# Kernel tuning notes

Hardware: AMD Instinct MI355X
Metric: run time of the kernel (lower is better)

Reference implementation:

```python
import jax, jax.numpy as jnp
import numpy as np
from jax import lax

SIGMA = 3.0
AP_CUT = 15


def _gauss_kernel(sigma, truncate=4.0):
    r = int(truncate * sigma + 0.5)
    x = np.arange(-r, r + 1, dtype=np.float32)
    k = np.exp(-0.5 * (x / sigma) ** 2)
    return jnp.asarray(k / k.sum()), r

KERN, RAD = _gauss_kernel(SIGMA)


def _smooth(f):
    """Separable Gaussian smoothing; circular on y (DV), replicate on x (AP).
    f: [..., Y, X] -> same shape."""
    lead = f.shape[:-2]
    Y, X = f.shape[-2:]
    g = f.reshape((-1, 1, Y, X))
    g = jnp.pad(g, ((0, 0), (0, 0), (RAD, RAD), (0, 0)), mode='wrap')
    g = jnp.pad(g, ((0, 0), (0, 0), (0, 0), (RAD, RAD)), mode='edge')
    ky = KERN.reshape(1, 1, -1, 1)
    kx = KERN.reshape(1, 1, 1, -1)
    g = lax.conv_general_dilated(g, ky, (1, 1), 'VALID')
    g = lax.conv_general_dilated(g, kx, (1, 1), 'VALID')
    return g.reshape(lead + (Y, X))


def _gradient(f):
    """Covariant gradient: Gaussian smooth then central differences.
    Returns [..., Y, X, 2] with index 0 = d/dy (circular), 1 = d/dx (replicate)."""
    g = _smooth(f)
    dy = 0.5 * (jnp.roll(g, -1, axis=-2) - jnp.roll(g, 1, axis=-2))
    gp = jnp.pad(g, [(0, 0)] * (g.ndim - 1) + [(1, 1)], mode='edge')
    dx = 0.5 * (gp[..., 2:] - gp[..., :-2])
    return jnp.stack([dy, dx], axis=-1)


def _postprocess(f):
    f = f.at[..., :AP_CUT].set(0.0)
    f = f.at[..., -AP_CUT:].set(0.0)
    return _smooth(f)


def setup_inputs() -> dict:
    key = jax.random.key(0)
    k1, k2 = jax.random.split(key)
    Y, X = 1024, 2048
    y = 0.1 * jax.random.normal(k1, (5, Y, X), dtype=jnp.float32)
    v = 0.1 * jax.random.normal(k2, (2, Y, X), dtype=jnp.float32)
    return {"y": y, "v": v}


def reference(y, v):
    Y, X = y.shape[-2:]
    # InputProcessor.transform: split state into 2x2 tensor m and scalar s
    m = y[:4].reshape(2, 2, Y, X)
    s = y[4]

    # get_velocity: left-right symmetrization (flip DV axis, negate y-component)
    v_lr = jnp.flip(v, axis=-2)
    v_lr = v_lr.at[0].multiply(-1.0)
    v = 0.5 * (v + v_lr)

    d1_m = _gradient(m)          # [2,2,Y,X,2]
    d1_s = _gradient(s)          # [Y,X,2]
    d1_v = _gradient(v)          # [2,Y,X,2]

    sdot = -jnp.einsum('iyx,yxi->yx', v, d1_s)

    T = jnp.transpose(d1_v, (0, 3, 1, 2))       # iyxj -> ijyx
    Tt = jnp.transpose(T, (1, 0, 2, 3))
    O = -0.5 * (T - Tt)                         # vorticity
    E = 0.5 * (T + Tt)                          # strain rate

    lhs = jnp.einsum('kyx,ijyxk->ijyx', v, d1_m)
    lhs = lhs + jnp.einsum('ikyx,kjyx->ijyx', O, m)
    lhs = lhs - jnp.einsum('ikyx,kjyx->ijyx', m, O)

    # rhs_eCad reaction terms
    trm = jnp.einsum('kkyx->yx', m)
    trE = jnp.einsum('kkyx->yx', E)
    gamma_dv = jnp.array([[1.0, 0.0], [0.0, 0.0]], dtype=y.dtype)[..., None, None]
    rhs = -(0.11 - 0.099 * s) * m
    rhs = rhs + (0.767 + 0.055 * s) * m * trE
    rhs = rhs + (0.732 - 0.59 * s) * trm * m
    rhs = rhs + (0.069 - 0.048 * s) * trm * gamma_dv

    mdot = _postprocess(-lhs + rhs)
    sdot = _postprocess(sdot)

    # inverse_transform: stack back into 5-channel state derivative
    return jnp.concatenate([mdot.reshape(4, Y, X), sdot[None]], axis=0)
```

## Files before the change

### kernel.cpp

```cpp
#include <hip/hip_runtime.h>
#include <math.h>

#define Y_ 1024
#define X_ 2048
#define YX_ (Y_*X_)
#define RAD_ 12
#define NT_ 25
#define ND_ 27
#define APC_ 15
#define PAD_ 16

struct W25 { float w[NT_]; };
struct D27 { float d[ND_]; };

__device__ __forceinline__ void wconv4(const float wb[36], const W25& W, float wc[4]) {
#pragma unroll
  for (int j = 0; j < 4; ++j) {
    float s = 0.f;
#pragma unroll
    for (int t = 0; t < NT_; ++t) s += W.w[t] * wb[4 + j + t];
    wc[j] = s;
  }
}
__device__ __forceinline__ void dconv4(const float wb[36], const D27& D, float dc[4]) {
#pragma unroll
  for (int j = 0; j < 4; ++j) {
    float s = 0.f;
#pragma unroll
    for (int t = 0; t < ND_; ++t) s += D.d[t] * wb[3 + j + t];
    dc[j] = s;
  }
}
__device__ __forceinline__ void load9(float wb[36], const float* p) {
#pragma unroll
  for (int i = 0; i < 9; ++i) {
    float4 t = *(const float4*)(p + 4 * i);
    wb[4*i+0] = t.x; wb[4*i+1] = t.y; wb[4*i+2] = t.z; wb[4*i+3] = t.w;
  }
}

__global__ __launch_bounds__(256) void ksmooth_y7c(
    const float* __restrict__ yin, const float* __restrict__ vin,
    float* __restrict__ out, W25 W)
{
  const int id = blockIdx.x;
  const int w  = (id & 7) * 112 + (id >> 3);
  const int yg = w % 64, xh = (w / 64) & 1, z = w / 128;
  const int y0 = yg * 16;
  const int xo = xh * 1024 + threadIdx.x * 4;

  float4 acc[16];
#pragma unroll
  for (int j = 0; j < 16; ++j) acc[j] = make_float4(0.f, 0.f, 0.f, 0.f);

  if (z < 5) {
    const float* base = yin + z * YX_;
#pragma unroll
    for (int g = 0; g < 4; ++g) {
      float4 b[10];
#pragma unroll
      for (int i = 0; i < 10; ++i) {
        const int r = (y0 - RAD_ + 10*g + i + Y_) & (Y_ - 1);
        b[i] = *(const float4*)(base + r * X_ + xo);
      }
#pragma unroll
      for (int i = 0; i < 10; ++i) {
        const int t = 10*g + i;
#pragma unroll
        for (int j = 0; j < 16; ++j) {
          const int k = t - j;
          if (k >= 0 && k < NT_) {
            const float wk = W.w[k];
            acc[j].x += wk * b[i].x; acc[j].y += wk * b[i].y;
            acc[j].z += wk * b[i].z; acc[j].w += wk * b[i].w;
          }
        }
      }
    }
  } else {
    const int   c   = z - 5;
    const float sgn = (c == 0) ? -1.f : 1.f;
    const float* base = vin + c * YX_;
#pragma unroll
    for (int g = 0; g < 8; ++g) {
      float4 a5[5], b5[5];
#pragma unroll
      for (int i = 0; i < 5; ++i) {
        const int r = (y0 - RAD_ + 5*g + i + Y_) & (Y_ - 1);
        a5[i] = *(const float4*)(base + r * X_ + xo);
        b5[i] = *(const float4*)(base + (Y_ - 1 - r) * X_ + xo);
      }
#pragma unroll
      for (int i = 0; i < 5; ++i) {
        const int t = 5*g + i;
        float4 val;
        val.x = 0.5f * (a5[i].x + sgn * b5[i].x);
        val.y = 0.5f * (a5[i].y + sgn * b5[i].y);
        val.z = 0.5f * (a5[i].z + sgn * b5[i].z);
        val.w = 0.5f * (a5[i].w + sgn * b5[i].w);
#pragma unroll
        for (int j = 0; j < 16; ++j) {
          const int k = t - j;
          if (k >= 0 && k < NT_) {
            const float wk = W.w[k];
            acc[j].x += wk * val.x; acc[j].y += wk * val.y;
            acc[j].z += wk * val.z; acc[j].w += wk * val.w;
          }
        }
      }
    }
  }
#pragma unroll
  for (int j = 0; j < 16; ++j)
    *(float4*)(out + z * YX_ + (y0 + j) * X_ + xo) = acc[j];
}

__global__ __launch_bounds__(256) void kderiv2(
    const float* __restrict__ gY, const float* __restrict__ vin,
    float* __restrict__ F, W25 W, D27 D)
{
  const int id = blockIdx.x;
  const int w  = (id & 7) * 224 + (id >> 3);
  const int yg = w % 128, xh = (w / 128) & 1, z = w / 256;
  const int y0 = yg * 8;
  const int x0 = xh * 1024 + threadIdx.x * 4;

  float w2[4], w1[4], dcp[4];
#pragma unroll
  for (int j = 0; j < 4; ++j) { w2[j] = 0.f; w1[j] = 0.f; dcp[j] = 0.f; }

  if (z < 5) {
    const float* base = gY + z * YX_;
#pragma unroll
    for (int r = 0; r < 10; ++r) {
      const int ry = (y0 - 1 + r + Y_) & (Y_ - 1);
      float wb[36];
      load9(wb, base + ry * X_ + x0 - 16);
      float wc[4]; wconv4(wb, W, wc);
      float dc[4];
      if (r >= 1 && r <= 8) dconv4(wb, D, dc);
      else { dc[0]=dc[1]=dc[2]=dc[3]=0.f; }
      if (r >= 2) {
        const int t = r - 2, ty = y0 + t;
        float4 a  = *(const float4*)(vin + 0*YX_ + ty * X_ + x0);
        float4 bm = *(const float4*)(vin + 0*YX_ + (Y_-1-ty) * X_ + x0);
        float4 c  = *(const float4*)(vin + 1*YX_ + ty * X_ + x0);
        float4 dm = *(const float4*)(vin + 1*YX_ + (Y_-1-ty) * X_ + x0);
        const float v0[4] = {0.5f*(a.x-bm.x), 0.5f*(a.y-bm.y),
                             0.5f*(a.z-bm.z), 0.5f*(a.w-bm.w)};
        const float v1[4] = {0.5f*(c.x+dm.x), 0.5f*(c.y+dm.y),
                             0.5f*(c.z+dm.z), 0.5f*(c.w+dm.w)};
        float4 o;
        o.x = v0[0]*(0.5f*(wc[0]-w2[0])) + v1[0]*dcp[0];
        o.y = v0[1]*(0.5f*(wc[1]-w2[1])) + v1[1]*dcp[1];
        o.z = v0[2]*(0.5f*(wc[2]-w2[2])) + v1[2]*dcp[2];
        o.w = v0[3]*(0.5f*(wc[3]-w2[3])) + v1[3]*dcp[3];
        *(float4*)(F + z * YX_ + ty * X_ + x0) = o;
      }
#pragma unroll
      for (int j = 0; j < 4; ++j) { w2[j] = w1[j]; w1[j] = wc[j]; dcp[j] = dc[j]; }
    }
  } else if (z == 5) {
    const float* b5 = gY + 5 * YX_;
    const float* b6 = gY + 6 * YX_;
#pragma unroll
    for (int r = 0; r < 10; ++r) {
      const int ry = (y0 - 1 + r + Y_) & (Y_ - 1);
      float wb[36];
      load9(wb, b6 + ry * X_ + x0 - 16);
      float wc[4]; wconv4(wb, W, wc);
      float dc[4];
      if (r >= 1 && r <= 8) {
        float wb5[36];
        load9(wb5, b5 + ry * X_ + x0 - 16);
        dconv4(wb5, D, dc);
      } else { dc[0]=dc[1]=dc[2]=dc[3]=0.f; }
      if (r >= 2) {
        const int t = r - 2, ty = y0 + t;
        float4 o;
        o.x = -0.5f*(dcp[0] - 0.5f*(wc[0]-w2[0]));
        o.y = -0.5f*(dcp[1] - 0.5f*(wc[1]-w2[1]));
        o.z = -0.5f*(dcp[2] - 0.5f*(wc[2]-w2[2]));
        o.w = -0.5f*(dcp[3] - 0.5f*(wc[3]-w2[3]));
        *(float4*)(F + 5 * YX_ + ty * X_ + x0) = o;
      }
#pragma unroll
      for (int j = 0; j < 4; ++j) { w2[j] = w1[j]; w1[j] = wc[j]; dcp[j] = dc[j]; }
    }
  } else {
    const float* b5 = gY + 5 * YX_;
    const float* b6 = gY + 6 * YX_;
#pragma unroll
    for (int r = 0; r < 10; ++r) {
      const int ry = (y0 - 1 + r + Y_) & (Y_ - 1);
      float wb[36];
      load9(wb, b5 + ry * X_ + x0 - 16);
      float wc[4]; wconv4(wb, W, wc);
      float dc[4];
      if (r >= 1 && r <= 8) {
        float wb6[36];
        load9(wb6, b6 + ry * X_ + x0 - 16);
        dconv4(wb6, D, dc);
      } else { dc[0]=dc[1]=dc[2]=dc[3]=0.f; }
      if (r >= 2) {
        const int t = r - 2, ty = y0 + t;
        float4 o;
        o.x = dcp[0] + 0.5f*(wc[0]-w2[0]);
        o.y = dcp[1] + 0.5f*(wc[1]-w2[1]);
        o.z = dcp[2] + 0.5f*(wc[2]-w2[2]);
        o.w = dcp[3] + 0.5f*(wc[3]-w2[3]);
        *(float4*)(F + 6 * YX_ + ty * X_ + x0) = o;
      }
#pragma unroll
      for (int j = 0; j < 4; ++j) { w2[j] = w1[j]; w1[j] = wc[j]; dcp[j] = dc[j]; }
    }
  }
}

__global__ __launch_bounds__(256) void kcombine(
    const float* __restrict__ F, const float* __restrict__ yin,
    float* __restrict__ B)
{
  const int yy = blockIdx.y;
  const int x0 = (blockIdx.x * 256 + threadIdx.x) * 4;

  if (x0 < RAD_ || x0 > X_ - PAD_) {
#pragma unroll
    for (int zc = 0; zc < 5; ++zc)
      *(float4*)(B + zc * YX_ + yy * X_ + x0) = make_float4(0.f,0.f,0.f,0.f);
    return;
  }

  float adv[5][4];
#pragma unroll
  for (int c = 0; c < 5; ++c) {
    float4 t = *(const float4*)(F + c * YX_ + yy * X_ + x0);
    adv[c][0] = t.x; adv[c][1] = t.y; adv[c][2] = t.z; adv[c][3] = t.w;
  }
  float4 wv  = *(const float4*)(F + 5 * YX_ + yy * X_ + x0);
  float4 tev = *(const float4*)(F + 6 * YX_ + yy * X_ + x0);
  const float wa[4]  = {wv.x, wv.y, wv.z, wv.w};
  const float tea[4] = {tev.x, tev.y, tev.z, tev.w};

  float rm[5][4];
#pragma unroll
  for (int zc = 0; zc < 5; ++zc) {
    float4 t = *(const float4*)(yin + zc * YX_ + yy * X_ + x0);
    rm[zc][0] = t.x; rm[zc][1] = t.y; rm[zc][2] = t.z; rm[zc][3] = t.w;
  }

  float o[5][4];
#pragma unroll
  for (int j = 0; j < 4; ++j) {
    const float m00r = rm[0][j], m01r = rm[1][j], m10r = rm[2][j], m11r = rm[3][j];
    const float sr   = rm[4][j];
    const float w_   = wa[j];
    const float trE  = tea[j];
    const float trm  = m00r + m11r;

    const float lhs00 = adv[0][j] + w_ * (m10r + m01r);
    const float lhs01 = adv[1][j] + w_ * (m11r - m00r);
    const float lhs10 = adv[2][j] + w_ * (m11r - m00r);
    const float lhs11 = adv[3][j] - w_ * (m01r + m10r);

    const float f  = -(0.11f - 0.099f * sr)
                   + (0.767f + 0.055f * sr) * trE
                   + (0.732f - 0.59f  * sr) * trm;
    const float cd = (0.069f - 0.048f * sr) * trm;
    const float sd = -adv[4][j];

    const int   xg   = x0 + j;
    const float mask = (xg < APC_ || xg >= X_ - APC_) ? 0.f : 1.f;
    o[0][j] = mask * (f * m00r + cd - lhs00);
    o[1][j] = mask * (f * m01r      - lhs01);
    o[2][j] = mask * (f * m10r      - lhs10);
    o[3][j] = mask * (f * m11r      - lhs11);
    o[4][j] = mask * sd;
  }
#pragma unroll
  for (int zc = 0; zc < 5; ++zc)
    *(float4*)(B + zc * YX_ + yy * X_ + x0) =
        make_float4(o[zc][0], o[zc][1], o[zc][2], o[zc][3]);
}

__global__ __launch_bounds__(256) void kxsmooth(
    const float* __restrict__ in, float* __restrict__ out, W25 W)
{
  const int z  = blockIdx.z;
  const int yy = blockIdx.y;
  const int x0 = (blockIdx.x * 256 + threadIdx.x) * 4;
  const float* row = in + z * YX_ + yy * X_;

  float buf[28];
  if (x0 >= RAD_ && x0 + 4 + RAD_ <= X_) {
#pragma unroll
    for (int i = 0; i < 7; ++i) {
      float4 t = *(const float4*)(row + x0 - RAD_ + 4 * i);
      buf[4*i+0] = t.x; buf[4*i+1] = t.y; buf[4*i+2] = t.z; buf[4*i+3] = t.w;
    }
  } else {
#pragma unroll
    for (int i = 0; i < 28; ++i) {
      int xx = x0 - RAD_ + i;
      xx = xx < 0 ? 0 : (xx > X_ - 1 ? X_ - 1 : xx);
      buf[i] = row[xx];
    }
  }
  float a0 = 0.f, a1 = 0.f, a2 = 0.f, a3 = 0.f;
#pragma unroll
  for (int t = 0; t < NT_; ++t) {
    const float wk = W.w[t];
    a0 += wk * buf[t + 0];
    a1 += wk * buf[t + 1];
    a2 += wk * buf[t + 2];
    a3 += wk * buf[t + 3];
  }
  *(float4*)(out + z * YX_ + yy * X_ + x0) = make_float4(a0, a1, a2, a3);
}

__global__ __launch_bounds__(256) void ksmooth_y5c(
    const float* __restrict__ in, float* __restrict__ out, W25 W)
{
  const int id = blockIdx.x;
  const int w  = (id & 7) * 80 + (id >> 3);
  const int yg = w % 64, xh = (w / 64) & 1, z = w / 128;
  const int y0 = yg * 16;
  const int xo = xh * 1024 + threadIdx.x * 4;
  const float* base = in + z * YX_;

  float4 acc[16];
#pragma unroll
  for (int j = 0; j < 16; ++j) acc[j] = make_float4(0.f, 0.f, 0.f, 0.f);

#pragma unroll
  for (int g = 0; g < 4; ++g) {
    float4 b[10];
#pragma unroll
    for (int i = 0; i < 10; ++i) {
      const int r = (y0 - RAD_ + 10*g + i + Y_) & (Y_ - 1);
      b[i] = *(const float4*)(base + r * X_ + xo);
    }
#pragma unroll
    for (int i = 0; i < 10; ++i) {
      const int t = 10*g + i;
#pragma unroll
      for (int j = 0; j < 16; ++j) {
        const int k = t - j;
        if (k >= 0 && k < NT_) {
          const float wk = W.w[k];
          acc[j].x += wk * b[i].x; acc[j].y += wk * b[i].y;
          acc[j].z += wk * b[i].z; acc[j].w += wk * b[i].w;
        }
      }
    }
  }
#pragma unroll
  for (int j = 0; j < 16; ++j)
    *(float4*)(out + z * YX_ + (y0 + j) * X_ + xo) = acc[j];
}

extern "C" void kernel_launch(void* const* d_in, const int* in_sizes, int n_in,
                              void* d_out, int out_size, void* d_ws, size_t ws_size,
                              hipStream_t stream)
{
  const float* yin = (const float*)d_in[0];
  const float* vin = (const float*)d_in[1];
  float* out = (float*)d_out;

  float* gY = (float*)d_ws + PAD_;
  float* F  = gY + 7 * (size_t)YX_;
  float* B  = F;
  float* C  = gY;

  W25 W; D27 D;
  double wd[NT_], s = 0.0;
  for (int i = 0; i < NT_; ++i) {
    const double x = i - RAD_;
    wd[i] = exp(-0.5 * (x / 3.0) * (x / 3.0));
    s += wd[i];
  }
  for (int i = 0; i < NT_; ++i) W.w[i] = (float)(wd[i] / s);
  for (int t = 0; t < ND_; ++t) {
    const double a = (t - 2 >= 0 && t - 2 < NT_) ? wd[t - 2] / s : 0.0;
    const double b = (t < NT_) ? wd[t] / s : 0.0;
    D.d[t] = (float)(0.5 * (a - b));
  }

  ksmooth_y7c<<<896, 256, 0, stream>>>(yin, vin, gY, W);
  kderiv2    <<<1792, 256, 0, stream>>>(gY, vin, F, W, D);
  kcombine   <<<dim3(2, 1024), 256, 0, stream>>>(F, yin, B);
  kxsmooth   <<<dim3(2, 1024, 5), 256, 0, stream>>>(B, C, W);
  ksmooth_y5c<<<640, 256, 0, stream>>>(C, out, W);
}
```

Baseline: 251.8 us.

## Fuse derivative and combine kernels into one per-row kernel

Merges the derivative kernel (kderiv2) and the combine kernel into a single kernel. Each thread now computes the x-smoothing and central differences for all seven channels directly from the y-smoothed buffer, instead of writing the intermediate F buffer and reading it back. This removes one launch and a full 7-channel intermediate round trip through memory. In exchange it recomputes the x-convolution for three rows per output row (up, down, centre) rather than sliding them along a row window, so arithmetic and redundant loads go up.

```diff
diff --git a/kernel.cpp b/kernel.cpp
--- a/kernel.cpp
+++ b/kernel.cpp
@@ -6,37 +6,55 @@
 #define YX_ (Y_*X_)
 #define RAD_ 12
 #define NT_ 25
-#define ND_ 27
 #define APC_ 15
 #define PAD_ 16
 
 struct W25 { float w[NT_]; };
-struct D27 { float d[ND_]; };
-
-__device__ __forceinline__ void wconv4(const float wb[36], const W25& W, float wc[4]) {
-#pragma unroll
-  for (int j = 0; j < 4; ++j) {
-    float s = 0.f;
-#pragma unroll
-    for (int t = 0; t < NT_; ++t) s += W.w[t] * wb[4 + j + t];
-    wc[j] = s;
-  }
-}
-__device__ __forceinline__ void dconv4(const float wb[36], const D27& D, float dc[4]) {
-#pragma unroll
-  for (int j = 0; j < 4; ++j) {
-    float s = 0.f;
-#pragma unroll
-    for (int t = 0; t < ND_; ++t) s += D.d[t] * wb[3 + j + t];
-    dc[j] = s;
-  }
-}
+
 __device__ __forceinline__ void load9(float wb[36], const float* p) {
 #pragma unroll
   for (int i = 0; i < 9; ++i) {
     float4 t = *(const float4*)(p + 4 * i);
     wb[4*i+0] = t.x; wb[4*i+1] = t.y; wb[4*i+2] = t.z; wb[4*i+3] = t.w;
   }
+}
+
+__device__ __forceinline__ void derivs_ch(
+    const float* __restrict__ base, int yy, int yu, int yd, int x0,
+    const W25& W, float dX[4], float dY[4])
+{
+  float wb[36];
+  load9(wb, base + yy * X_ + x0 - 16);
+  float wc6[6];
+#pragma unroll
+  for (int jj = 0; jj < 6; ++jj) {
+    float s = 0.f;
+#pragma unroll
+    for (int t = 0; t < NT_; ++t) s += W.w[t] * wb[3 + jj + t];
+    wc6[jj] = s;
+  }
+#pragma unroll
+  for (int j = 0; j < 4; ++j) dX[j] = 0.5f * (wc6[j + 2] - wc6[j]);
+
+  float au[4], ad[4];
+  load9(wb, base + yu * X_ + x0 - 16);
+#pragma unroll
+  for (int j = 0; j < 4; ++j) {
+    float s = 0.f;
+#pragma unroll
+    for (int t = 0; t < NT_; ++t) s += W.w[t] * wb[4 + j + t];
+    au[j] = s;
+  }
+  load9(wb, base + yd * X_ + x0 - 16);
+#pragma unroll
+  for (int j = 0; j < 4; ++j) {
+    float s = 0.f;
+#pragma unroll
+    for (int t = 0; t < NT_; ++t) s += W.w[t] * wb[4 + j + t];
+    ad[j] = s;
+  }
+#pragma unroll
+  for (int j = 0; j < 4; ++j) dY[j] = 0.5f * (au[j] - ad[j]);
 }
 
 __global__ __launch_bounds__(256) void ksmooth_y7c(
@@ -115,114 +133,18 @@
     *(float4*)(out + z * YX_ + (y0 + j) * X_ + xo) = acc[j];
 }
 
-__global__ __launch_bounds__(256) void kderiv2(
-    const float* __restrict__ gY, const float* __restrict__ vin,
-    float* __restrict__ F, W25 W, D27 D)
+__global__ __launch_bounds__(256) void kfused(
+    const float* __restrict__ gY,
+    const float* __restrict__ yin,
+    const float* __restrict__ vin,
+    float* __restrict__ B,
+    W25 W)
 {
   const int id = blockIdx.x;
-  const int w  = (id & 7) * 224 + (id >> 3);
-  const int yg = w % 128, xh = (w / 128) & 1, z = w / 256;
-  const int y0 = yg * 8;
+  const int w  = (id & 7) * 256 + (id >> 3);
+  const int yy = w & (Y_ - 1);
+  const int xh = w >> 10;
   const int x0 = xh * 1024 + threadIdx.x * 4;
-
-  float w2[4], w1[4], dcp[4];
-#pragma unroll
-  for (int j = 0; j < 4; ++j) { w2[j] = 0.f; w1[j] = 0.f; dcp[j] = 0.f; }
-
-  if (z < 5) {
-    const float* base = gY + z * YX_;
-#pragma unroll
-    for (int r = 0; r < 10; ++r) {
-      const int ry = (y0 - 1 + r + Y_) & (Y_ - 1);
-      float wb[36];
-      load9(wb, base + ry * X_ + x0 - 16);
-      float wc[4]; wconv4(wb, W, wc);
-      float dc[4];
-      if (r >= 1 && r <= 8) dconv4(wb, D, dc);
-      else { dc[0]=dc[1]=dc[2]=dc[3]=0.f; }
-      if (r >= 2) {
-        const int t = r - 2, ty = y0 + t;
-        float4 a  = *(const float4*)(vin + 0*YX_ + ty * X_ + x0);
-        float4 bm = *(const float4*)(vin + 0*YX_ + (Y_-1-ty) * X_ + x0);
-        float4 c  = *(const float4*)(vin + 1*YX_ + ty * X_ + x0);
-        float4 dm = *(const float4*)(vin + 1*YX_ + (Y_-1-ty) * X_ + x0);
-        const float v0[4] = {0.5f*(a.x-bm.x), 0.5f*(a.y-bm.y),
-                             0.5f*(a.z-bm.z), 0.5f*(a.w-bm.w)};
-        const float v1[4] = {0.5f*(c.x+dm.x), 0.5f*(c.y+dm.y),
-                             0.5f*(c.z+dm.z), 0.5f*(c.w+dm.w)};
-        float4 o;
-        o.x = v0[0]*(0.5f*(wc[0]-w2[0])) + v1[0]*dcp[0];
-        o.y = v0[1]*(0.5f*(wc[1]-w2[1])) + v1[1]*dcp[1];
-        o.z = v0[2]*(0.5f*(wc[2]-w2[2])) + v1[2]*dcp[2];
-        o.w = v0[3]*(0.5f*(wc[3]-w2[3])) + v1[3]*dcp[3];
-        *(float4*)(F + z * YX_ + ty * X_ + x0) = o;
-      }
-#pragma unroll
-      for (int j = 0; j < 4; ++j) { w2[j] = w1[j]; w1[j] = wc[j]; dcp[j] = dc[j]; }
-    }
-  } else if (z == 5) {
-    const float* b5 = gY + 5 * YX_;
-    const float* b6 = gY + 6 * YX_;
-#pragma unroll
-    for (int r = 0; r < 10; ++r) {
-      const int ry = (y0 - 1 + r + Y_) & (Y_ - 1);
-      float wb[36];
-      load9(wb, b6 + ry * X_ + x0 - 16);
-      float wc[4]; wconv4(wb, W, wc);
-      float dc[4];
-      if (r >= 1 && r <= 8) {
-        float wb5[36];
-        load9(wb5, b5 + ry * X_ + x0 - 16);
-        dconv4(wb5, D, dc);
-      } else { dc[0]=dc[1]=dc[2]=dc[3]=0.f; }
-      if (r >= 2) {
-        const int t = r - 2, ty = y0 + t;
-        float4 o;
-        o.x = -0.5f*(dcp[0] - 0.5f*(wc[0]-w2[0]));
-        o.y = -0.5f*(dcp[1] - 0.5f*(wc[1]-w2[1]));
-        o.z = -0.5f*(dcp[2] - 0.5f*(wc[2]-w2[2]));
-        o.w = -0.5f*(dcp[3] - 0.5f*(wc[3]-w2[3]));
-        *(float4*)(F + 5 * YX_ + ty * X_ + x0) = o;
-      }
-#pragma unroll
-      for (int j = 0; j < 4; ++j) { w2[j] = w1[j]; w1[j] = wc[j]; dcp[j] = dc[j]; }
-    }
-  } else {
-    const float* b5 = gY + 5 * YX_;
-    const float* b6 = gY + 6 * YX_;
-#pragma unroll
-    for (int r = 0; r < 10; ++r) {
-      const int ry = (y0 - 1 + r + Y_) & (Y_ - 1);
-      float wb[36];
-      load9(wb, b5 + ry * X_ + x0 - 16);
-      float wc[4]; wconv4(wb, W, wc);
-      float dc[4];
-      if (r >= 1 && r <= 8) {
-        float wb6[36];
-        load9(wb6, b6 + ry * X_ + x0 - 16);
-        dconv4(wb6, D, dc);
-      } else { dc[0]=dc[1]=dc[2]=dc[3]=0.f; }
-      if (r >= 2) {
-        const int t = r - 2, ty = y0 + t;
-        float4 o;
-        o.x = dcp[0] + 0.5f*(wc[0]-w2[0]);
-        o.y = dcp[1] + 0.5f*(wc[1]-w2[1]);
-        o.z = dcp[2] + 0.5f*(wc[2]-w2[2]);
-        o.w = dcp[3] + 0.5f*(wc[3]-w2[3]);
-        *(float4*)(F + 6 * YX_ + ty * X_ + x0) = o;
-      }
-#pragma unroll
-      for (int j = 0; j < 4; ++j) { w2[j] = w1[j]; w1[j] = wc[j]; dcp[j] = dc[j]; }
-    }
-  }
-}
-
-__global__ __launch_bounds__(256) void kcombine(
-    const float* __restrict__ F, const float* __restrict__ yin,
-    float* __restrict__ B)
-{
-  const int yy = blockIdx.y;
-  const int x0 = (blockIdx.x * 256 + threadIdx.x) * 4;
 
   if (x0 < RAD_ || x0 > X_ - PAD_) {
 #pragma unroll
@@ -231,16 +153,41 @@
     return;
   }
 
-  float adv[5][4];
+  const int yu = (yy + 1) & (Y_ - 1);
+  const int yd = (yy - 1) & (Y_ - 1);
+
+  float v0[4], v1[4];
+  {
+    float4 a = *(const float4*)(vin + 0 * YX_ + yy * X_ + x0);
+    float4 b = *(const float4*)(vin + 0 * YX_ + (Y_ - 1 - yy) * X_ + x0);
+    float4 c = *(const float4*)(vin + 1 * YX_ + yy * X_ + x0);
+    float4 d = *(const float4*)(vin + 1 * YX_ + (Y_ - 1 - yy) * X_ + x0);
+    v0[0] = 0.5f*(a.x-b.x); v0[1] = 0.5f*(a.y-b.y);
+    v0[2] = 0.5f*(a.z-b.z); v0[3] = 0.5f*(a.w-b.w);
+    v1[0] = 0.5f*(c.x+d.x); v1[1] = 0.5f*(c.y+d.y);
+    v1[2] = 0.5f*(c.z+d.z); v1[3] = 0.5f*(c.w+d.w);
+  }
+
+  float w_[4], trE[4];
+  {
+    float dX5[4], dY5[4], dX6[4], dY6[4];
+    derivs_ch(gY + 5 * YX_, yy, yu, yd, x0, W, dX5, dY5);
+    derivs_ch(gY + 6 * YX_, yy, yu, yd, x0, W, dX6, dY6);
+#pragma unroll
+    for (int j = 0; j < 4; ++j) {
+      w_[j]  = -0.5f * (dX5[j] - dY6[j]);
+      trE[j] = dY5[j] + dX6[j];
+    }
+  }
+
+  float acc[5][4];
 #pragma unroll
   for (int c = 0; c < 5; ++c) {
-    float4 t = *(const float4*)(F + c * YX_ + yy * X_ + x0);
-    adv[c][0] = t.x; adv[c][1] = t.y; adv[c][2] = t.z; adv[c][3] = t.w;
-  }
-  float4 wv  = *(const float4*)(F + 5 * YX_ + yy * X_ + x0);
-  float4 tev = *(const float4*)(F + 6 * YX_ + yy * X_ + x0);
-  const float wa[4]  = {wv.x, wv.y, wv.z, wv.w};
-  const float tea[4] = {tev.x, tev.y, tev.z, tev.w};
+    float dX[4], dY[4];
+    derivs_ch(gY + c * YX_, yy, yu, yd, x0, W, dX, dY);
+#pragma unroll
+    for (int j = 0; j < 4; ++j) acc[c][j] = v0[j] * dY[j] + v1[j] * dX[j];
+  }
 
   float rm[5][4];
 #pragma unroll
@@ -254,20 +201,19 @@
   for (int j = 0; j < 4; ++j) {
     const float m00r = rm[0][j], m01r = rm[1][j], m10r = rm[2][j], m11r = rm[3][j];
     const float sr   = rm[4][j];
-    const float w_   = wa[j];
-    const float trE  = tea[j];
+    const float wj   = w_[j];
     const float trm  = m00r + m11r;
 
-    const float lhs00 = adv[0][j] + w_ * (m10r + m01r);
-    const float lhs01 = adv[1][j] + w_ * (m11r - m00r);
-    const float lhs10 = adv[2][j] + w_ * (m11r - m00r);
-    const float lhs11 = adv[3][j] - w_ * (m01r + m10r);
+    const float lhs00 = acc[0][j] + wj * (m10r + m01r);
+    const float lhs01 = acc[1][j] + wj * (m11r - m00r);
+    const float lhs10 = acc[2][j] + wj * (m11r - m00r);
+    const float lhs11 = acc[3][j] - wj * (m01r + m10r);
 
     const float f  = -(0.11f - 0.099f * sr)
-                   + (0.767f + 0.055f * sr) * trE
+                   + (0.767f + 0.055f * sr) * trE[j]
                    + (0.732f - 0.59f  * sr) * trm;
     const float cd = (0.069f - 0.048f * sr) * trm;
-    const float sd = -adv[4][j];
+    const float sd = -acc[4][j];
 
     const int   xg   = x0 + j;
     const float mask = (xg < APC_ || xg >= X_ - APC_) ? 0.f : 1.f;
@@ -368,11 +314,10 @@
   float* out = (float*)d_out;
 
   float* gY = (float*)d_ws + PAD_;
-  float* F  = gY + 7 * (size_t)YX_;
-  float* B  = F;
+  float* B  = gY + 7 * (size_t)YX_;
   float* C  = gY;
 
-  W25 W; D27 D;
+  W25 W;
   double wd[NT_], s = 0.0;
   for (int i = 0; i < NT_; ++i) {
     const double x = i - RAD_;
@@ -380,15 +325,9 @@
     s += wd[i];
   }
   for (int i = 0; i < NT_; ++i) W.w[i] = (float)(wd[i] / s);
-  for (int t = 0; t < ND_; ++t) {
-    const double a = (t - 2 >= 0 && t - 2 < NT_) ? wd[t - 2] / s : 0.0;
-    const double b = (t < NT_) ? wd[t] / s : 0.0;
-    D.d[t] = (float)(0.5 * (a - b));
-  }
-
-  ksmooth_y7c<<<896, 256, 0, stream>>>(yin, vin, gY, W);
-  kderiv2    <<<1792, 256, 0, stream>>>(gY, vin, F, W, D);
-  kcombine   <<<dim3(2, 1024), 256, 0, stream>>>(F, yin, B);
+
+  ksmooth_y7c<<<896,  256, 0, stream>>>(yin, vin, gY, W);
+  kfused     <<<2048, 256, 0, stream>>>(gY, yin, vin, B, W);
   kxsmooth   <<<dim3(2, 1024, 5), 256, 0, stream>>>(B, C, W);
-  ksmooth_y5c<<<640, 256, 0, stream>>>(C, out, W);
-}
+  ksmooth_y5c<<<640,  256, 0, stream>>>(C, out, W);
+}
```

After: 224.3 us. 1.12x faster.
